# Kernel tuning notes

Measured on AMD Instinct MI355X. Metric: run time of the kernel, lower is better.

The kernel has to match this reference:

```python
import jax, jax.numpy as jnp
import numpy as np

B, S, H, L = 2, 192, 768, 4

def setup_inputs() -> dict:
    key = jax.random.key(0)
    ks = jax.random.split(key, 6)
    scale = 1.0 / np.sqrt(H)
    return {
        "pooled": jax.random.normal(ks[0], (B, S, H), dtype=jnp.float32),
        "W_src": jax.random.normal(ks[1], (H * L, H), dtype=jnp.float32) * scale,
        "b_src": jax.random.normal(ks[2], (H * L,), dtype=jnp.float32) * 0.02,
        "W_tgt": jax.random.normal(ks[3], (H * L, H), dtype=jnp.float32) * scale,
        "b_tgt": jax.random.normal(ks[4], (H * L,), dtype=jnp.float32) * 0.02,
        "classifier_weight": jax.random.normal(ks[5], (H, L), dtype=jnp.float32) * scale,
    }

def reference(pooled, W_src, b_src, W_tgt, b_tgt, classifier_weight):
    b, s, h = pooled.shape
    l = classifier_weight.shape[1]
    # Linear projections: (b,s,h) @ (h, L*h) -> (b,s,L,h)
    h_source = (pooled @ W_src.T + b_src).reshape(b, s, l, h)
    h_target = (pooled @ W_tgt.T + b_tgt).reshape(b, s, l, h)
    # Pairwise broadcast-add -> (b,s,t,l,h), exact (erf) GELU as in nn.GELU()
    hidden = jax.nn.gelu(h_source[:, :, None] + h_target[:, None], approximate=False)
    # dropout is identity at inference
    return jnp.einsum('bstlh,hl->bstl', hidden, classifier_weight)
```

## Files before the change

kernel.cpp:

```cpp
#include <hip/hip_runtime.h>
#include <math.h>

#define BQ 2
#define SQ 192
#define HQ 768
#define LQ 4

typedef float f32x4 __attribute__((ext_vector_type(4)));
typedef short bf16x8 __attribute__((ext_vector_type(8)));

__device__ __forceinline__ float gelu_f(float x) {
  float ax = fabsf(x);
  float q = fmaf(fmaf(fmaf(fmaf(0.0232217f, ax, 0.00040867f), ax, 0.1369901f),
                      ax, 0.2340973f), ax, 1.18920712f);
  float r  = __builtin_amdgcn_rcpf(q);
  float r2 = r * r;
  float r4 = r2 * r2;
  return fmaf(-ax, r4, fmaxf(x, 0.f));
}

__device__ __forceinline__ unsigned short bf16_rne(float x) {
  unsigned u = __float_as_uint(x);
  return (unsigned short)((u + 0x7fffu + ((u >> 16) & 1u)) >> 16);
}

__global__ __launch_bounds__(256) void prep_kernel(
    const float* __restrict__ pooled, const float* __restrict__ Ws,
    const float* __restrict__ Wt, const float* __restrict__ cw,
    unsigned short* __restrict__ Ab, unsigned short* __restrict__ Wsb,
    unsigned short* __restrict__ Wtb, float* __restrict__ clp)
{
  int blk = blockIdx.x;
  if (blk >= 408) {
    int i = (blk - 408) * 256 + threadIdx.x;
    clp[i] = cw[(i % HQ) * LQ + i / HQ];
    return;
  }
  const float* src; unsigned short* dst; int rt;
  if (blk < 24)       { src = pooled; dst = Ab;  rt = blk; }
  else if (blk < 216) { src = Ws;     dst = Wsb; rt = blk - 24; }
  else                { src = Wt;     dst = Wtb; rt = blk - 216; }

  #pragma unroll
  for (int i = 0; i < 6; ++i) {
    int c    = threadIdx.x + i * 256;
    int kt   = c >> 6;
    int lane = c & 63;
    int row  = rt * 16 + (lane & 15);
    int col  = kt * 32 + (lane >> 4) * 8;
    const float* s = src + (size_t)row * HQ + col;
    float4 v0 = *(const float4*)s;
    float4 v1 = *(const float4*)(s + 4);
    ushort4 o0, o1;
    o0.x = bf16_rne(v0.x); o0.y = bf16_rne(v0.y);
    o0.z = bf16_rne(v0.z); o0.w = bf16_rne(v0.w);
    o1.x = bf16_rne(v1.x); o1.y = bf16_rne(v1.y);
    o1.z = bf16_rne(v1.z); o1.w = bf16_rne(v1.w);
    unsigned short* d = dst + ((size_t)(rt * 24 + kt) * 64 + lane) * 8;
    *(ushort4*)d       = o0;
    *(ushort4*)(d + 4) = o1;
  }
}

__global__ __launch_bounds__(64) void proj_mfma(
    const unsigned short* __restrict__ APk,
    const unsigned short* __restrict__ WsPk, const unsigned short* __restrict__ WtPk,
    const float* __restrict__ b0, const float* __restrict__ b1,
    float* __restrict__ o0, float* __restrict__ o1)
{
  int id  = blockIdx.x + 12 * (blockIdx.y + 96 * blockIdx.z);
  int nid = (id & 7) * 288 + (id >> 3);
  int bm = nid % 12, bn = (nid / 12) % 96, bz = nid / 1152;

  const unsigned short* WPk = bz ? WtPk : WsPk;
  const float* bias = bz ? b1 : b0;
  float* out        = bz ? o1 : o0;

  int lane = threadIdx.x;
  int m_base = bm * 32, n_base = bn * 32;

  const unsigned short* a0p = APk + (size_t)(bm * 2) * 24 * 512 + lane * 8;
  const unsigned short* a1p = a0p + 24 * 512;
  const unsigned short* w0p = WPk + (size_t)(bn * 2) * 24 * 512 + lane * 8;
  const unsigned short* w1p = w0p + 24 * 512;

  f32x4 acc00 = {0,0,0,0}, acc01 = {0,0,0,0}, acc10 = {0,0,0,0}, acc11 = {0,0,0,0};

  bf16x8 a0 = *(const bf16x8*)a0p, a1 = *(const bf16x8*)a1p;
  bf16x8 v0 = *(const bf16x8*)w0p, v1 = *(const bf16x8*)w1p;
  for (int kt = 0; kt < 23; ++kt) {
    int off = (kt + 1) * 512;
    bf16x8 na0 = *(const bf16x8*)(a0p + off), na1 = *(const bf16x8*)(a1p + off);
    bf16x8 nv0 = *(const bf16x8*)(w0p + off), nv1 = *(const bf16x8*)(w1p + off);
    acc00 = __builtin_amdgcn_mfma_f32_16x16x32_bf16(a0, v0, acc00, 0, 0, 0);
    acc01 = __builtin_amdgcn_mfma_f32_16x16x32_bf16(a0, v1, acc01, 0, 0, 0);
    acc10 = __builtin_amdgcn_mfma_f32_16x16x32_bf16(a1, v0, acc10, 0, 0, 0);
    acc11 = __builtin_amdgcn_mfma_f32_16x16x32_bf16(a1, v1, acc11, 0, 0, 0);
    a0 = na0; a1 = na1; v0 = nv0; v1 = nv1;
  }
  acc00 = __builtin_amdgcn_mfma_f32_16x16x32_bf16(a0, v0, acc00, 0, 0, 0);
  acc01 = __builtin_amdgcn_mfma_f32_16x16x32_bf16(a0, v1, acc01, 0, 0, 0);
  acc10 = __builtin_amdgcn_mfma_f32_16x16x32_bf16(a1, v0, acc10, 0, 0, 0);
  acc11 = __builtin_amdgcn_mfma_f32_16x16x32_bf16(a1, v1, acc11, 0, 0, 0);

  int l      = n_base / HQ;
  int h_base = n_base % HQ;
  int bb     = m_base / SQ;
  int c      = lane & 15, g = lane >> 4;
  float bv0 = bias[n_base + c];
  float bv1 = bias[n_base + 16 + c];
  #pragma unroll
  for (int i = 0; i < 2; ++i) {
    f32x4 A0 = i ? acc10 : acc00;
    f32x4 A1 = i ? acc11 : acc01;
    #pragma unroll
    for (int reg = 0; reg < 4; ++reg) {
      int m = m_base + i * 16 + g * 4 + reg;
      int s = m - bb * SQ;
      float* op = out + (((size_t)(bb * LQ + l) * SQ + s) * HQ) + h_base;
      op[c]      = A0[reg] + bv0;
      op[16 + c] = A1[reg] + bv1;
    }
  }
}

__global__ __launch_bounds__(256) void proj_kernel(
    const float* __restrict__ A,
    const float* __restrict__ W0, const float* __restrict__ b0,
    const float* __restrict__ W1, const float* __restrict__ b1,
    float* __restrict__ o0, float* __restrict__ o1)
{
  const float* W  = blockIdx.z ? W1 : W0;
  const float* bs = blockIdx.z ? b1 : b0;
  float* out      = blockIdx.z ? o1 : o0;

  __shared__ float As[32][68];
  __shared__ float Wt[64][68];

  const int tid = threadIdx.x;
  const int tx  = tid & 15;
  const int ty  = tid >> 4;
  const int m0  = blockIdx.x * 32;
  const int n0  = blockIdx.y * 64;

  const int ar[2] = { (tid + 0) >> 4, (tid + 256) >> 4 };
  const int ac    = (tid & 15) << 2;
  const int wr[4] = { tid >> 4, (tid + 256) >> 4, (tid + 512) >> 4, (tid + 768) >> 4 };
  const int wc    = (tid & 15) << 2;

  float4 pa[2], pw[4];
  #pragma unroll
  for (int i = 0; i < 2; ++i)
    pa[i] = *(const float4*)&A[(size_t)(m0 + ar[i]) * HQ + ac];
  #pragma unroll
  for (int i = 0; i < 4; ++i)
    pw[i] = *(const float4*)&W[(size_t)(n0 + wr[i]) * HQ + wc];

  float acc[2][4];
  #pragma unroll
  for (int j = 0; j < 2; ++j)
    #pragma unroll
    for (int n = 0; n < 4; ++n) acc[j][n] = 0.f;

  for (int kt = 0; kt < 12; ++kt) {
    __syncthreads();
    #pragma unroll
    for (int i = 0; i < 2; ++i)
      *(float4*)&As[ar[i]][ac] = pa[i];
    #pragma unroll
    for (int i = 0; i < 4; ++i) {
      Wt[wc + 0][wr[i]] = pw[i].x; Wt[wc + 1][wr[i]] = pw[i].y;
      Wt[wc + 2][wr[i]] = pw[i].z; Wt[wc + 3][wr[i]] = pw[i].w;
    }
    if (kt < 11) {
      int ko = (kt + 1) * 64;
      #pragma unroll
      for (int i = 0; i < 2; ++i)
        pa[i] = *(const float4*)&A[(size_t)(m0 + ar[i]) * HQ + ko + ac];
      #pragma unroll
      for (int i = 0; i < 4; ++i)
        pw[i] = *(const float4*)&W[(size_t)(n0 + wr[i]) * HQ + ko + wc];
    }
    __syncthreads();

    #pragma unroll
    for (int kk = 0; kk < 64; kk += 4) {
      float4 a[2], wv[4];
      #pragma unroll
      for (int j = 0; j < 2; ++j)
        a[j] = *(float4*)&As[2 * ty + j][kk];
      #pragma unroll
      for (int i = 0; i < 4; ++i)
        wv[i] = *(float4*)&Wt[kk + i][4 * tx];
      #pragma unroll
      for (int i = 0; i < 4; ++i) {
        #pragma unroll
        for (int j = 0; j < 2; ++j) {
          float av = ((const float*)&a[j])[i];
          acc[j][0] = fmaf(av, wv[i].x, acc[j][0]);
          acc[j][1] = fmaf(av, wv[i].y, acc[j][1]);
          acc[j][2] = fmaf(av, wv[i].z, acc[j][2]);
          acc[j][3] = fmaf(av, wv[i].w, acc[j][3]);
        }
      }
    }
  }

  const int l  = n0 / HQ;
  const int h0 = n0 % HQ;
  float4 bv = *(const float4*)&bs[n0 + 4 * tx];
  #pragma unroll
  for (int j = 0; j < 2; ++j) {
    int m  = m0 + 2 * ty + j;
    int bb = m / SQ, s = m % SQ;
    float4 v;
    v.x = acc[j][0] + bv.x; v.y = acc[j][1] + bv.y;
    v.z = acc[j][2] + bv.z; v.w = acc[j][3] + bv.w;
    *(float4*)(out + (((size_t)(bb * LQ + l) * SQ + s) * HQ) + h0 + 4 * tx) = v;
  }
}

__global__ __launch_bounds__(256) void pack_kernel(const float* __restrict__ cw,
                                                   float* __restrict__ clp) {
  int i = blockIdx.x * 256 + threadIdx.x;
  int l = i / HQ, h = i % HQ;
  clp[i] = cw[h * LQ + l];
}

__global__ __launch_bounds__(256, 8) void pair_kernel(
    const float* __restrict__ hsrc, const float* __restrict__ htgt,
    const float* __restrict__ clp, float* __restrict__ out)
{
  int id  = blockIdx.x + 12 * (blockIdx.y + 12 * blockIdx.z);
  int nid = (id & 7) * 144 + (id >> 3);
  int bix = nid % 12, biy = (nid / 12) % 12, bl = nid / 144;

  const int bb = bl >> 2, l = bl & 3;
  const int s0 = bix * 16;
  const int t0 = biy * 16;
  const int tid = threadIdx.x;
  const int tt = tid & 15;
  const int ts = tid >> 4;

  __shared__ float htile[16][256];

  const float* hs_row = hsrc + ((size_t)bl * SQ + s0 + ts) * HQ;
  const float* ht_g   = htgt + ((size_t)bl * SQ + t0) * HQ;
  const float* clp_l  = clp + l * HQ;

  const int tsw = (tt & 7) << 2;

  float acc = 0.f;
  for (int ck = 0; ck < 3; ++ck) {
    __syncthreads();
    #pragma unroll
    for (int i = 0; i < 4; ++i) {
      int f4 = tid + i * 256;
      int r  = f4 >> 6;
      int cq = (f4 & 63) << 2;
      float4 v = *(const float4*)&ht_g[(size_t)r * HQ + ck * 256 + cq];
      *(float4*)&htile[r][cq ^ ((r & 7) << 2)] = v;
    }
    __syncthreads();

    #pragma unroll 4
    for (int k = 0; k < 256; k += 4) {
      float4 a  = *(const float4*)&hs_row[ck * 256 + k];
      float4 b  = *(float4*)&htile[tt][k ^ tsw];
      float4 c4 = *(const float4*)&clp_l[ck * 256 + k];
      acc = fmaf(gelu_f(a.x + b.x), c4.x, acc);
      acc = fmaf(gelu_f(a.y + b.y), c4.y, acc);
      acc = fmaf(gelu_f(a.z + b.z), c4.z, acc);
      acc = fmaf(gelu_f(a.w + b.w), c4.w, acc);
    }
  }

  out[(((size_t)bb * SQ + (s0 + ts)) * SQ + (t0 + tt)) * LQ + l] = acc;
}

extern "C" void kernel_launch(void* const* d_in, const int* in_sizes, int n_in,
                              void* d_out, int out_size, void* d_ws, size_t ws_size,
                              hipStream_t stream) {
  const float* pooled = (const float*)d_in[0];
  const float* Wsrc   = (const float*)d_in[1];
  const float* bsrc   = (const float*)d_in[2];
  const float* Wtgt   = (const float*)d_in[3];
  const float* btgt   = (const float*)d_in[4];
  const float* cw     = (const float*)d_in[5];
  float* out = (float*)d_out;

  const size_t nhs = (size_t)BQ * LQ * SQ * HQ;
  float* clp = (float*)d_ws;
  float* hs  = clp + LQ * HQ;
  float* ht  = hs + nhs;
  unsigned short* Ab  = (unsigned short*)(ht + nhs);
  unsigned short* Wsb = Ab + (size_t)BQ * SQ * HQ;
  unsigned short* Wtb = Wsb + (size_t)LQ * HQ * HQ;

  size_t need_full = (size_t)(LQ * HQ + 2 * nhs) * 4 +
                     (size_t)(BQ * SQ * HQ + 2 * LQ * HQ * HQ) * 2;

  if (ws_size >= need_full) {
    prep_kernel<<<dim3(420), 256, 0, stream>>>(pooled, Wsrc, Wtgt, cw, Ab, Wsb, Wtb, clp);
    proj_mfma<<<dim3(12, 96, 2), 64, 0, stream>>>(Ab, Wsb, Wtb, bsrc, btgt, hs, ht);
  } else {
    pack_kernel<<<dim3(12), 256, 0, stream>>>(cw, clp);
    proj_kernel<<<dim3(12, 48, 2), 256, 0, stream>>>(pooled, Wsrc, bsrc, Wtgt, btgt, hs, ht);
  }
  pair_kernel<<<dim3(12, 12, 8), 256, 0, stream>>>(hs, ht, clp, out);
}
```

Before: 174.2 us.

## Store projections as bf16, stage both tiles in LDS, vectorize GELU pairwise

The projection outputs are now written as bf16, which halves the intermediate traffic. The pair kernel stages both the source and target tiles in LDS as fp32, in 128-wide chunks. The GELU and accumulate step runs on float2 vectors so the compiler can emit packed FMA instructions, and occupancy drops from 8 to 4 blocks per SM. Separately, the prep kernel is split into one sub-chunk per block for more parallelism, and the MFMA loop is unrolled two-deep. Rounding hsrc and htgt to bf16 adds error before the GELU sum.

```diff
diff --git a/kernel.cpp b/kernel.cpp
--- a/kernel.cpp
+++ b/kernel.cpp
@@ -6,22 +6,32 @@
 #define HQ 768
 #define LQ 4
 
-typedef float f32x4 __attribute__((ext_vector_type(4)));
-typedef short bf16x8 __attribute__((ext_vector_type(8)));
-
-__device__ __forceinline__ float gelu_f(float x) {
-  float ax = fabsf(x);
-  float q = fmaf(fmaf(fmaf(fmaf(0.0232217f, ax, 0.00040867f), ax, 0.1369901f),
-                      ax, 0.2340973f), ax, 1.18920712f);
-  float r  = __builtin_amdgcn_rcpf(q);
-  float r2 = r * r;
-  float r4 = r2 * r2;
-  return fmaf(-ax, r4, fmaxf(x, 0.f));
+typedef float  f2     __attribute__((ext_vector_type(2)));
+typedef float  f32x4  __attribute__((ext_vector_type(4)));
+typedef short  bf16x8 __attribute__((ext_vector_type(8)));
+typedef unsigned short u16x8 __attribute__((ext_vector_type(8)));
+
+__device__ __forceinline__ f2 gelu2(f2 x) {
+  f2 ax = __builtin_elementwise_abs(x);
+  f2 q  = __builtin_elementwise_fma((f2)0.0232217f, ax, (f2)0.00040867f);
+  q     = __builtin_elementwise_fma(q, ax, (f2)0.1369901f);
+  q     = __builtin_elementwise_fma(q, ax, (f2)0.2340973f);
+  q     = __builtin_elementwise_fma(q, ax, (f2)1.18920712f);
+  f2 r;
+  r.x = __builtin_amdgcn_rcpf(q.x);
+  r.y = __builtin_amdgcn_rcpf(q.y);
+  f2 r2 = r * r;
+  f2 r4 = r2 * r2;
+  f2 relu = __builtin_elementwise_max(x, (f2)0.0f);
+  return __builtin_elementwise_fma(-ax, r4, relu);
 }
 
 __device__ __forceinline__ unsigned short bf16_rne(float x) {
   unsigned u = __float_as_uint(x);
   return (unsigned short)((u + 0x7fffu + ((u >> 16) & 1u)) >> 16);
+}
+__device__ __forceinline__ float b2f(unsigned short u) {
+  return __uint_as_float((unsigned)u << 16);
 }
 
 __global__ __launch_bounds__(256) void prep_kernel(
@@ -31,42 +41,40 @@
     unsigned short* __restrict__ Wtb, float* __restrict__ clp)
 {
   int blk = blockIdx.x;
-  if (blk >= 408) {
-    int i = (blk - 408) * 256 + threadIdx.x;
+  if (blk >= 2448) {
+    int i = (blk - 2448) * 256 + threadIdx.x;
     clp[i] = cw[(i % HQ) * LQ + i / HQ];
     return;
   }
+  int unit = blk / 6, sub = blk % 6;
   const float* src; unsigned short* dst; int rt;
-  if (blk < 24)       { src = pooled; dst = Ab;  rt = blk; }
-  else if (blk < 216) { src = Ws;     dst = Wsb; rt = blk - 24; }
-  else                { src = Wt;     dst = Wtb; rt = blk - 216; }
-
-  #pragma unroll
-  for (int i = 0; i < 6; ++i) {
-    int c    = threadIdx.x + i * 256;
-    int kt   = c >> 6;
-    int lane = c & 63;
-    int row  = rt * 16 + (lane & 15);
-    int col  = kt * 32 + (lane >> 4) * 8;
-    const float* s = src + (size_t)row * HQ + col;
-    float4 v0 = *(const float4*)s;
-    float4 v1 = *(const float4*)(s + 4);
-    ushort4 o0, o1;
-    o0.x = bf16_rne(v0.x); o0.y = bf16_rne(v0.y);
-    o0.z = bf16_rne(v0.z); o0.w = bf16_rne(v0.w);
-    o1.x = bf16_rne(v1.x); o1.y = bf16_rne(v1.y);
-    o1.z = bf16_rne(v1.z); o1.w = bf16_rne(v1.w);
-    unsigned short* d = dst + ((size_t)(rt * 24 + kt) * 64 + lane) * 8;
-    *(ushort4*)d       = o0;
-    *(ushort4*)(d + 4) = o1;
-  }
+  if (unit < 24)       { src = pooled; dst = Ab;  rt = unit; }
+  else if (unit < 216) { src = Ws;     dst = Wsb; rt = unit - 24; }
+  else                 { src = Wt;     dst = Wtb; rt = unit - 216; }
+
+  int c    = threadIdx.x + sub * 256;
+  int kt   = c >> 6;
+  int lane = c & 63;
+  int row  = rt * 16 + (lane & 15);
+  int col  = kt * 32 + (lane >> 4) * 8;
+  const float* s = src + (size_t)row * HQ + col;
+  float4 v0 = *(const float4*)s;
+  float4 v1 = *(const float4*)(s + 4);
+  ushort4 o0, o1;
+  o0.x = bf16_rne(v0.x); o0.y = bf16_rne(v0.y);
+  o0.z = bf16_rne(v0.z); o0.w = bf16_rne(v0.w);
+  o1.x = bf16_rne(v1.x); o1.y = bf16_rne(v1.y);
+  o1.z = bf16_rne(v1.z); o1.w = bf16_rne(v1.w);
+  unsigned short* d = dst + ((size_t)(rt * 24 + kt) * 64 + lane) * 8;
+  *(ushort4*)d       = o0;
+  *(ushort4*)(d + 4) = o1;
 }
 
 __global__ __launch_bounds__(64) void proj_mfma(
     const unsigned short* __restrict__ APk,
     const unsigned short* __restrict__ WsPk, const unsigned short* __restrict__ WtPk,
     const float* __restrict__ b0, const float* __restrict__ b1,
-    float* __restrict__ o0, float* __restrict__ o1)
+    unsigned short* __restrict__ o0, unsigned short* __restrict__ o1)
 {
   int id  = blockIdx.x + 12 * (blockIdx.y + 96 * blockIdx.z);
   int nid = (id & 7) * 288 + (id >> 3);
@@ -74,7 +82,7 @@
 
   const unsigned short* WPk = bz ? WtPk : WsPk;
   const float* bias = bz ? b1 : b0;
-  float* out        = bz ? o1 : o0;
+  unsigned short* out = bz ? o1 : o0;
 
   int lane = threadIdx.x;
   int m_base = bm * 32, n_base = bn * 32;
@@ -86,22 +94,38 @@
 
   f32x4 acc00 = {0,0,0,0}, acc01 = {0,0,0,0}, acc10 = {0,0,0,0}, acc11 = {0,0,0,0};
 
-  bf16x8 a0 = *(const bf16x8*)a0p, a1 = *(const bf16x8*)a1p;
-  bf16x8 v0 = *(const bf16x8*)w0p, v1 = *(const bf16x8*)w1p;
-  for (int kt = 0; kt < 23; ++kt) {
-    int off = (kt + 1) * 512;
-    bf16x8 na0 = *(const bf16x8*)(a0p + off), na1 = *(const bf16x8*)(a1p + off);
-    bf16x8 nv0 = *(const bf16x8*)(w0p + off), nv1 = *(const bf16x8*)(w1p + off);
-    acc00 = __builtin_amdgcn_mfma_f32_16x16x32_bf16(a0, v0, acc00, 0, 0, 0);
-    acc01 = __builtin_amdgcn_mfma_f32_16x16x32_bf16(a0, v1, acc01, 0, 0, 0);
-    acc10 = __builtin_amdgcn_mfma_f32_16x16x32_bf16(a1, v0, acc10, 0, 0, 0);
-    acc11 = __builtin_amdgcn_mfma_f32_16x16x32_bf16(a1, v1, acc11, 0, 0, 0);
-    a0 = na0; a1 = na1; v0 = nv0; v1 = nv1;
-  }
-  acc00 = __builtin_amdgcn_mfma_f32_16x16x32_bf16(a0, v0, acc00, 0, 0, 0);
-  acc01 = __builtin_amdgcn_mfma_f32_16x16x32_bf16(a0, v1, acc01, 0, 0, 0);
-  acc10 = __builtin_amdgcn_mfma_f32_16x16x32_bf16(a1, v0, acc10, 0, 0, 0);
-  acc11 = __builtin_amdgcn_mfma_f32_16x16x32_bf16(a1, v1, acc11, 0, 0, 0);
+  bf16x8 A0 = *(const bf16x8*)a0p,        A1 = *(const bf16x8*)a1p;
+  bf16x8 U0 = *(const bf16x8*)w0p,        U1 = *(const bf16x8*)w1p;
+  bf16x8 B0 = *(const bf16x8*)(a0p+512),  B1 = *(const bf16x8*)(a1p+512);
+  bf16x8 X0 = *(const bf16x8*)(w0p+512),  X1 = *(const bf16x8*)(w1p+512);
+
+  #pragma unroll
+  for (int it = 0; it < 11; ++it) {
+    int offA = (2 * it + 2) * 512;
+    int offB = (2 * it + 3) * 512;
+    bf16x8 nA0 = *(const bf16x8*)(a0p + offA), nA1 = *(const bf16x8*)(a1p + offA);
+    bf16x8 nU0 = *(const bf16x8*)(w0p + offA), nU1 = *(const bf16x8*)(w1p + offA);
+    acc00 = __builtin_amdgcn_mfma_f32_16x16x32_bf16(A0, U0, acc00, 0, 0, 0);
+    acc01 = __builtin_amdgcn_mfma_f32_16x16x32_bf16(A0, U1, acc01, 0, 0, 0);
+    acc10 = __builtin_amdgcn_mfma_f32_16x16x32_bf16(A1, U0, acc10, 0, 0, 0);
+    acc11 = __builtin_amdgcn_mfma_f32_16x16x32_bf16(A1, U1, acc11, 0, 0, 0);
+    A0 = nA0; A1 = nA1; U0 = nU0; U1 = nU1;
+    bf16x8 nB0 = *(const bf16x8*)(a0p + offB), nB1 = *(const bf16x8*)(a1p + offB);
+    bf16x8 nX0 = *(const bf16x8*)(w0p + offB), nX1 = *(const bf16x8*)(w1p + offB);
+    acc00 = __builtin_amdgcn_mfma_f32_16x16x32_bf16(B0, X0, acc00, 0, 0, 0);
+    acc01 = __builtin_amdgcn_mfma_f32_16x16x32_bf16(B0, X1, acc01, 0, 0, 0);
+    acc10 = __builtin_amdgcn_mfma_f32_16x16x32_bf16(B1, X0, acc10, 0, 0, 0);
+    acc11 = __builtin_amdgcn_mfma_f32_16x16x32_bf16(B1, X1, acc11, 0, 0, 0);
+    B0 = nB0; B1 = nB1; X0 = nX0; X1 = nX1;
+  }
+  acc00 = __builtin_amdgcn_mfma_f32_16x16x32_bf16(A0, U0, acc00, 0, 0, 0);
+  acc01 = __builtin_amdgcn_mfma_f32_16x16x32_bf16(A0, U1, acc01, 0, 0, 0);
+  acc10 = __builtin_amdgcn_mfma_f32_16x16x32_bf16(A1, U0, acc10, 0, 0, 0);
+  acc11 = __builtin_amdgcn_mfma_f32_16x16x32_bf16(A1, U1, acc11, 0, 0, 0);
+  acc00 = __builtin_amdgcn_mfma_f32_16x16x32_bf16(B0, X0, acc00, 0, 0, 0);
+  acc01 = __builtin_amdgcn_mfma_f32_16x16x32_bf16(B0, X1, acc01, 0, 0, 0);
+  acc10 = __builtin_amdgcn_mfma_f32_16x16x32_bf16(B1, X0, acc10, 0, 0, 0);
+  acc11 = __builtin_amdgcn_mfma_f32_16x16x32_bf16(B1, X1, acc11, 0, 0, 0);
 
   int l      = n_base / HQ;
   int h_base = n_base % HQ;
@@ -111,15 +135,15 @@
   float bv1 = bias[n_base + 16 + c];
   #pragma unroll
   for (int i = 0; i < 2; ++i) {
-    f32x4 A0 = i ? acc10 : acc00;
-    f32x4 A1 = i ? acc11 : acc01;
+    f32x4 C0 = i ? acc10 : acc00;
+    f32x4 C1 = i ? acc11 : acc01;
     #pragma unroll
     for (int reg = 0; reg < 4; ++reg) {
       int m = m_base + i * 16 + g * 4 + reg;
       int s = m - bb * SQ;
-      float* op = out + (((size_t)(bb * LQ + l) * SQ + s) * HQ) + h_base;
-      op[c]      = A0[reg] + bv0;
-      op[16 + c] = A1[reg] + bv1;
+      unsigned short* op = out + (((size_t)(bb * LQ + l) * SQ + s) * HQ) + h_base;
+      op[c]      = bf16_rne(C0[reg] + bv0);
+      op[16 + c] = bf16_rne(C1[reg] + bv1);
     }
   }
 }
@@ -128,11 +152,11 @@
     const float* __restrict__ A,
     const float* __restrict__ W0, const float* __restrict__ b0,
     const float* __restrict__ W1, const float* __restrict__ b1,
-    float* __restrict__ o0, float* __restrict__ o1)
+    unsigned short* __restrict__ o0, unsigned short* __restrict__ o1)
 {
   const float* W  = blockIdx.z ? W1 : W0;
   const float* bs = blockIdx.z ? b1 : b0;
-  float* out      = blockIdx.z ? o1 : o0;
+  unsigned short* out = blockIdx.z ? o1 : o0;
 
   __shared__ float As[32][68];
   __shared__ float Wt[64][68];
@@ -213,10 +237,10 @@
   for (int j = 0; j < 2; ++j) {
     int m  = m0 + 2 * ty + j;
     int bb = m / SQ, s = m % SQ;
-    float4 v;
-    v.x = acc[j][0] + bv.x; v.y = acc[j][1] + bv.y;
-    v.z = acc[j][2] + bv.z; v.w = acc[j][3] + bv.w;
-    *(float4*)(out + (((size_t)(bb * LQ + l) * SQ + s) * HQ) + h0 + 4 * tx) = v;
+    ushort4 v;
+    v.x = bf16_rne(acc[j][0] + bv.x); v.y = bf16_rne(acc[j][1] + bv.y);
+    v.z = bf16_rne(acc[j][2] + bv.z); v.w = bf16_rne(acc[j][3] + bv.w);
+    *(ushort4*)(out + (((size_t)(bb * LQ + l) * SQ + s) * HQ) + h0 + 4 * tx) = v;
   }
 }
 
@@ -227,8 +251,8 @@
   clp[i] = cw[h * LQ + l];
 }
 
-__global__ __launch_bounds__(256, 8) void pair_kernel(
-    const float* __restrict__ hsrc, const float* __restrict__ htgt,
+__global__ __launch_bounds__(256, 4) void pair_kernel(
+    const unsigned short* __restrict__ hsrc, const unsigned short* __restrict__ htgt,
     const float* __restrict__ clp, float* __restrict__ out)
 {
   int id  = blockIdx.x + 12 * (blockIdx.y + 12 * blockIdx.z);
@@ -242,40 +266,49 @@
   const int tt = tid & 15;
   const int ts = tid >> 4;
 
-  __shared__ float htile[16][256];
-
-  const float* hs_row = hsrc + ((size_t)bl * SQ + s0 + ts) * HQ;
-  const float* ht_g   = htgt + ((size_t)bl * SQ + t0) * HQ;
-  const float* clp_l  = clp + l * HQ;
-
-  const int tsw = (tt & 7) << 2;
-
-  float acc = 0.f;
-  for (int ck = 0; ck < 3; ++ck) {
+  __shared__ float hstile[16][132];
+  __shared__ float httile[16][132];
+
+  const unsigned short* hs_g = hsrc + ((size_t)bl * SQ + s0) * HQ;
+  const unsigned short* ht_g = htgt + ((size_t)bl * SQ + t0) * HQ;
+  const float* clp_l = clp + l * HQ;
+
+  const int srow = tid >> 4;
+  const int scol = (tid & 15) * 8;
+
+  f2 acc = {0.f, 0.f};
+  #pragma unroll 1
+  for (int ck = 0; ck < 6; ++ck) {
     __syncthreads();
-    #pragma unroll
-    for (int i = 0; i < 4; ++i) {
-      int f4 = tid + i * 256;
-      int r  = f4 >> 6;
-      int cq = (f4 & 63) << 2;
-      float4 v = *(const float4*)&ht_g[(size_t)r * HQ + ck * 256 + cq];
-      *(float4*)&htile[r][cq ^ ((r & 7) << 2)] = v;
+    {
+      u16x8 uh = *(const u16x8*)&hs_g[(size_t)srow * HQ + ck * 128 + scol];
+      u16x8 ut = *(const u16x8*)&ht_g[(size_t)srow * HQ + ck * 128 + scol];
+      float4 f0, f1, g0, g1;
+      f0.x = b2f(uh[0]); f0.y = b2f(uh[1]); f0.z = b2f(uh[2]); f0.w = b2f(uh[3]);
+      f1.x = b2f(uh[4]); f1.y = b2f(uh[5]); f1.z = b2f(uh[6]); f1.w = b2f(uh[7]);
+      g0.x = b2f(ut[0]); g0.y = b2f(ut[1]); g0.z = b2f(ut[2]); g0.w = b2f(ut[3]);
+      g1.x = b2f(ut[4]); g1.y = b2f(ut[5]); g1.z = b2f(ut[6]); g1.w = b2f(ut[7]);
+      *(float4*)&hstile[srow][scol]     = f0;
+      *(float4*)&hstile[srow][scol + 4] = f1;
+      *(float4*)&httile[srow][scol]     = g0;
+      *(float4*)&httile[srow][scol + 4] = g1;
     }
     __syncthreads();
 
     #pragma unroll 4
-    for (int k = 0; k < 256; k += 4) {
-      float4 a  = *(const float4*)&hs_row[ck * 256 + k];
-      float4 b  = *(float4*)&htile[tt][k ^ tsw];
-      float4 c4 = *(const float4*)&clp_l[ck * 256 + k];
-      acc = fmaf(gelu_f(a.x + b.x), c4.x, acc);
-      acc = fmaf(gelu_f(a.y + b.y), c4.y, acc);
-      acc = fmaf(gelu_f(a.z + b.z), c4.z, acc);
-      acc = fmaf(gelu_f(a.w + b.w), c4.w, acc);
-    }
-  }
-
-  out[(((size_t)bb * SQ + (s0 + ts)) * SQ + (t0 + tt)) * LQ + l] = acc;
+    for (int k = 0; k < 128; k += 4) {
+      float4 a  = *(float4*)&hstile[ts][k];
+      float4 b  = *(float4*)&httile[tt][k];
+      float4 c4 = *(const float4*)&clp_l[ck * 128 + k];
+      const f2* ap = (const f2*)&a;
+      const f2* bp = (const f2*)&b;
+      const f2* cp = (const f2*)&c4;
+      acc = __builtin_elementwise_fma(gelu2(ap[0] + bp[0]), cp[0], acc);
+      acc = __builtin_elementwise_fma(gelu2(ap[1] + bp[1]), cp[1], acc);
+    }
+  }
+
+  out[(((size_t)bb * SQ + (s0 + ts)) * SQ + (t0 + tt)) * LQ + l] = acc.x + acc.y;
 }
 
 extern "C" void kernel_launch(void* const* d_in, const int* in_sizes, int n_in,
@@ -291,21 +324,21 @@
 
   const size_t nhs = (size_t)BQ * LQ * SQ * HQ;
   float* clp = (float*)d_ws;
-  float* hs  = clp + LQ * HQ;
-  float* ht  = hs + nhs;
-  unsigned short* Ab  = (unsigned short*)(ht + nhs);
+  unsigned short* hsb = (unsigned short*)(clp + LQ * HQ);
+  unsigned short* htb = hsb + nhs;
+  unsigned short* Ab  = htb + nhs;
   unsigned short* Wsb = Ab + (size_t)BQ * SQ * HQ;
   unsigned short* Wtb = Wsb + (size_t)LQ * HQ * HQ;
 
-  size_t need_full = (size_t)(LQ * HQ + 2 * nhs) * 4 +
+  size_t need_full = (size_t)(LQ * HQ) * 4 + 2 * nhs * 2 +
                      (size_t)(BQ * SQ * HQ + 2 * LQ * HQ * HQ) * 2;
 
   if (ws_size >= need_full) {
-    prep_kernel<<<dim3(420), 256, 0, stream>>>(pooled, Wsrc, Wtgt, cw, Ab, Wsb, Wtb, clp);
-    proj_mfma<<<dim3(12, 96, 2), 64, 0, stream>>>(Ab, Wsb, Wtb, bsrc, btgt, hs, ht);
+    prep_kernel<<<dim3(2460), 256, 0, stream>>>(pooled, Wsrc, Wtgt, cw, Ab, Wsb, Wtb, clp);
+    proj_mfma<<<dim3(12, 96, 2), 64, 0, stream>>>(Ab, Wsb, Wtb, bsrc, btgt, hsb, htb);
   } else {
     pack_kernel<<<dim3(12), 256, 0, stream>>>(cw, clp);
-    proj_kernel<<<dim3(12, 48, 2), 256, 0, stream>>>(pooled, Wsrc, bsrc, Wtgt, btgt, hs, ht);
-  }
-  pair_kernel<<<dim3(12, 12, 8), 256, 0, stream>>>(hs, ht, clp, out);
-}
+    proj_kernel<<<dim3(12, 48, 2), 256, 0, stream>>>(pooled, Wsrc, bsrc, Wtgt, btgt, hsb, htb);
+  }
+  pair_kernel<<<dim3(12, 12, 8), 256, 0, stream>>>(hsb, htb, clp, out);
+}
```

After: 155.6 us. 1.12x faster.
